# Performance work log

Hardware: AMD Instinct MI355X
Metric: run time of the kernel (lower is better)

The kernel has to match this reference:

```python
import jax, jax.numpy as jnp
import numpy as np

B, N, DIN, DOUT, EIN, EOUT = 8, 256, 64, 64, 64, 64


def setup_inputs() -> dict:
    key = jax.random.key(0)
    ks = jax.random.split(key, 9)
    A = jax.random.randint(ks[0], (B, N, N), 0, 2).astype(jnp.float32)  # {0,1} connectivity
    emb_node = jax.random.normal(ks[1], (B, N, DIN), dtype=jnp.float32)
    emb_edge = jax.random.normal(ks[2], (B, N, N, EIN), dtype=jnp.float32)
    s_n = 1.0 / np.sqrt(DIN)
    s_e = 1.0 / np.sqrt(EIN)
    Wn = jax.random.uniform(ks[3], (DIN, DOUT), minval=-s_n, maxval=s_n)
    bn = jax.random.uniform(ks[4], (DOUT,), minval=-s_n, maxval=s_n)
    Wsn = jax.random.uniform(ks[5], (DIN, DOUT), minval=-s_n, maxval=s_n)
    bsn = jax.random.uniform(ks[6], (DOUT,), minval=-s_n, maxval=s_n)
    We = jax.random.uniform(ks[7], (EIN, EOUT), minval=-s_e, maxval=s_e)
    be = jax.random.uniform(ks[8], (EOUT,), minval=-s_e, maxval=s_e)
    return {"A": A, "emb_node": emb_node, "emb_edge": emb_edge,
            "Wn": Wn, "bn": bn, "Wsn": Wsn, "bsn": bsn, "We": We, "be": be}


def reference(A, emb_node, emb_edge, Wn, bn, Wsn, bsn, We, be):
    # mode=1 (default) of ChannelIndependentConv
    node_x = emb_node @ Wn + bn          # [B,N,DOUT]
    node_sx = emb_node @ Wsn + bsn       # [B,N,DOUT]
    edge_x = emb_edge @ We + be          # [B,N,N,EOUT]
    # mask edges by connectivity, then channel-independent aggregation:
    # out[b,i,c] = sum_j A[b,i,j] * edge_x[b,i,j,c] * node_x[b,j,c]
    Ae = A[..., None] * edge_x           # [B,N,N,EOUT]
    agg = jnp.einsum('bijc,bjc->bic', Ae, node_x)  # [B,N,DOUT]
    node_out = jax.nn.relu(agg) + jax.nn.relu(node_sx)
    edge_out = jax.nn.relu(edge_x)
    return node_out, edge_out
```

## Files before the change

kernel.cpp:

```cpp
#include <hip/hip_runtime.h>
#include <hip/hip_bf16.h>

#define BN   2048
#define NN   256
#define CH   64

typedef __attribute__((ext_vector_type(8))) short short8;
typedef __attribute__((ext_vector_type(4))) float fv4;

static __device__ inline short f2bf(float f) {
  unsigned u = __float_as_uint(f);
  u += 0x7FFF + ((u >> 16) & 1);
  return (short)(u >> 16);
}
static __device__ inline short8 cvt8(fv4 a, fv4 b) {
  short8 f;
  f[0] = f2bf(a[0]); f[1] = f2bf(a[1]); f[2] = f2bf(a[2]); f[3] = f2bf(a[3]);
  f[4] = f2bf(b[0]); f[5] = f2bf(b[1]); f[6] = f2bf(b[2]); f[7] = f2bf(b[3]);
  return f;
}

__global__ __launch_bounds__(256) void node_kernel(
    const float* __restrict__ emb_node, const float* __restrict__ Wn,
    const float* __restrict__ bn, const float* __restrict__ Wsn,
    const float* __restrict__ bsn, float* __restrict__ node_x,
    float* __restrict__ rsx) {
  __shared__ float s_emb[4][CH];
  __shared__ float s_Wn[CH * CH];
  __shared__ float s_Ws[CH * CH];
  const int tid = threadIdx.x;
  const int r = tid >> 6;
  const int c = tid & 63;
  const int row = blockIdx.x * 4 + r;
#pragma unroll
  for (int i = 0; i < 4; ++i) {
    *(fv4*)&s_Wn[(i * 256 + tid) * 4] = *(const fv4*)&Wn[(i * 256 + tid) * 4];
    *(fv4*)&s_Ws[(i * 256 + tid) * 4] = *(const fv4*)&Wsn[(i * 256 + tid) * 4];
  }
  s_emb[r][c] = emb_node[row * CH + c];
  __syncthreads();
  float a1 = bn[c], a2 = bsn[c];
#pragma unroll
  for (int k = 0; k < CH; ++k) {
    const float e = s_emb[r][k];
    a1 = fmaf(e, s_Wn[k * CH + c], a1);
    a2 = fmaf(e, s_Ws[k * CH + c], a2);
  }
  node_x[row * CH + c] = a1;
  rsx[row * CH + c] = fmaxf(a2, 0.0f);
}

__global__ __launch_bounds__(256) void edge_mfma_kernel(
    const float* __restrict__ A, const float* __restrict__ emb_edge,
    const float* __restrict__ We, const float* __restrict__ be,
    const float* __restrict__ node_x, const float* __restrict__ rsx,
    float* __restrict__ node_out, float* __restrict__ edge_out) {
  const int bi   = blockIdx.x;
  const int b    = bi >> 8;
  const int tid  = threadIdx.x;
  const int lane = tid & 63;
  const int wave = tid >> 6;
  const int l15  = lane & 15;
  const int quad = lane >> 4;

  __shared__ float s_A[NN];
  __shared__ float s_agg[CH];

  s_A[tid] = A[(size_t)bi * NN + tid];
  if (tid < CH) s_agg[tid] = 0.0f;

  short8 bfrag[4][2];
  float bias[4];
#pragma unroll
  for (int ct = 0; ct < 4; ++ct) {
    const int c = 16 * ct + l15;
#pragma unroll
    for (int h = 0; h < 2; ++h)
#pragma unroll
      for (int j = 0; j < 8; ++j)
        bfrag[ct][h][j] = f2bf(We[(h * 32 + quad * 8 + j) * CH + c]);
    bias[ct] = be[c];
  }

  const float* __restrict__ ee = emb_edge + (size_t)bi * NN * CH;
  float*       __restrict__ eo = edge_out + (size_t)bi * NN * CH;
  const float* __restrict__ nx = node_x + (size_t)b * NN * CH;

  const int jbase = wave * 64;
  __syncthreads();

  fv4 ld[2][4];
#pragma unroll
  for (int q = 0; q < 4; ++q) {
    const float* p = ee + (size_t)(jbase + l15) * CH + quad * 8 + (q & 1) * 4 + (q >> 1) * 32;
    ld[0][q] = __builtin_nontemporal_load((const fv4*)p);
  }

  float agg[4] = {0.0f, 0.0f, 0.0f, 0.0f};

#pragma unroll
  for (int t = 0; t < 4; ++t) {
    const int pb = t & 1;
    if (t < 3) {
#pragma unroll
      for (int q = 0; q < 4; ++q) {
        const float* p = ee + (size_t)(jbase + (t + 1) * 16 + l15) * CH +
                         quad * 8 + (q & 1) * 4 + (q >> 1) * 32;
        ld[pb ^ 1][q] = __builtin_nontemporal_load((const fv4*)p);
      }
    }
    const int rbase = jbase + t * 16 + quad * 4;
    float nxv[4][4];
#pragma unroll
    for (int ct = 0; ct < 4; ++ct)
#pragma unroll
      for (int r = 0; r < 4; ++r)
        nxv[ct][r] = nx[(rbase + r) * CH + 16 * ct + l15];

    const short8 af0 = cvt8(ld[pb][0], ld[pb][1]);
    const short8 af1 = cvt8(ld[pb][2], ld[pb][3]);
    fv4 acc[4];
#pragma unroll
    for (int ct = 0; ct < 4; ++ct) {
      acc[ct] = fv4{0.0f, 0.0f, 0.0f, 0.0f};
      acc[ct] = __builtin_amdgcn_mfma_f32_16x16x32_bf16(af0, bfrag[ct][0], acc[ct], 0, 0, 0);
      acc[ct] = __builtin_amdgcn_mfma_f32_16x16x32_bf16(af1, bfrag[ct][1], acc[ct], 0, 0, 0);
    }

    const fv4 av = *(const fv4*)&s_A[rbase];
#pragma unroll
    for (int ct = 0; ct < 4; ++ct) {
      const int c = 16 * ct + l15;
#pragma unroll
      for (int r = 0; r < 4; ++r) {
        const float ex = acc[ct][r] + bias[ct];
        __builtin_nontemporal_store(fmaxf(ex, 0.0f), eo + (rbase + r) * CH + c);
        agg[ct] = fmaf(av[r] * ex, nxv[ct][r], agg[ct]);
      }
    }
  }

#pragma unroll
  for (int ct = 0; ct < 4; ++ct) {
    agg[ct] += __shfl_xor(agg[ct], 16, 64);
    agg[ct] += __shfl_xor(agg[ct], 32, 64);
  }
  if (quad == 0) {
#pragma unroll
    for (int ct = 0; ct < 4; ++ct)
      atomicAdd(&s_agg[16 * ct + l15], agg[ct]);
  }
  __syncthreads();
  if (tid < CH) {
    node_out[(size_t)bi * CH + tid] =
        fmaxf(s_agg[tid], 0.0f) + rsx[(size_t)bi * CH + tid];
  }
}

extern "C" void kernel_launch(void* const* d_in, const int* in_sizes, int n_in,
                              void* d_out, int out_size, void* d_ws, size_t ws_size,
                              hipStream_t stream) {
  const float* A        = (const float*)d_in[0];
  const float* emb_node = (const float*)d_in[1];
  const float* emb_edge = (const float*)d_in[2];
  const float* Wn       = (const float*)d_in[3];
  const float* bn       = (const float*)d_in[4];
  const float* Wsn      = (const float*)d_in[5];
  const float* bsn      = (const float*)d_in[6];
  const float* We       = (const float*)d_in[7];
  const float* be       = (const float*)d_in[8];

  float* node_out = (float*)d_out;
  float* edge_out = (float*)d_out + (size_t)BN * CH;

  float* node_x = (float*)d_ws;
  float* rsx    = (float*)d_ws + (size_t)BN * CH;

  hipLaunchKernelGGL(node_kernel, dim3(BN / 4), dim3(256), 0, stream,
                     emb_node, Wn, bn, Wsn, bsn, node_x, rsx);
  hipLaunchKernelGGL(edge_mfma_kernel, dim3(BN), dim3(256), 0, stream,
                     A, emb_edge, We, be, node_x, rsx, node_out, edge_out);
}
```

Before: 269.0 us.

## Deepen edge load prefetch, hoist loads before weight setup, and truncate bf16 via perm

Issues the first two 16-row tiles of edge embeddings and the first node_x tile before the We/bias fragment setup and the barrier, so more memory traffic is in flight early. The edge prefetch distance grows from one tile to two, and node_x rows are double-buffered one tile ahead. The float-to-bf16 conversion switches from round-to-nearest-even to byte-permute truncation, which uses fewer ALU ops but loses the rounding step and slightly lowers accuracy. Register use goes up with the extra buffers.

```diff
diff --git a/kernel.cpp b/kernel.cpp
--- a/kernel.cpp
+++ b/kernel.cpp
@@ -13,11 +13,14 @@
   u += 0x7FFF + ((u >> 16) & 1);
   return (short)(u >> 16);
 }
-static __device__ inline short8 cvt8(fv4 a, fv4 b) {
-  short8 f;
-  f[0] = f2bf(a[0]); f[1] = f2bf(a[1]); f[2] = f2bf(a[2]); f[3] = f2bf(a[3]);
-  f[4] = f2bf(b[0]); f[5] = f2bf(b[1]); f[6] = f2bf(b[2]); f[7] = f2bf(b[3]);
-  return f;
+
+static __device__ inline short8 pk8(fv4 a, fv4 b) {
+  union { short8 s; unsigned u[4]; } r;
+  r.u[0] = __builtin_amdgcn_perm(__float_as_uint(a[1]), __float_as_uint(a[0]), 0x07060302u);
+  r.u[1] = __builtin_amdgcn_perm(__float_as_uint(a[3]), __float_as_uint(a[2]), 0x07060302u);
+  r.u[2] = __builtin_amdgcn_perm(__float_as_uint(b[1]), __float_as_uint(b[0]), 0x07060302u);
+  r.u[3] = __builtin_amdgcn_perm(__float_as_uint(b[3]), __float_as_uint(b[2]), 0x07060302u);
+  return r.s;
 }
 
 __global__ __launch_bounds__(256) void node_kernel(
@@ -69,6 +72,28 @@
   s_A[tid] = A[(size_t)bi * NN + tid];
   if (tid < CH) s_agg[tid] = 0.0f;
 
+  const float* __restrict__ ee = emb_edge + (size_t)bi * NN * CH;
+  float*       __restrict__ eo = edge_out + (size_t)bi * NN * CH;
+  const float* __restrict__ nx = node_x + (size_t)b * NN * CH;
+  const int jbase = wave * 64;
+
+  fv4 ld[4][4];
+#pragma unroll
+  for (int t = 0; t < 2; ++t)
+#pragma unroll
+    for (int q = 0; q < 4; ++q) {
+      const float* p = ee + (size_t)(jbase + t * 16 + l15) * CH +
+                       quad * 8 + (q & 1) * 4 + (q >> 1) * 32;
+      ld[t][q] = __builtin_nontemporal_load((const fv4*)p);
+    }
+
+  float nxv[2][4][4];
+#pragma unroll
+  for (int ct = 0; ct < 4; ++ct)
+#pragma unroll
+    for (int r = 0; r < 4; ++r)
+      nxv[0][ct][r] = nx[(jbase + quad * 4 + r) * CH + 16 * ct + l15];
+
   short8 bfrag[4][2];
   float bias[4];
 #pragma unroll
@@ -82,43 +107,30 @@
     bias[ct] = be[c];
   }
 
-  const float* __restrict__ ee = emb_edge + (size_t)bi * NN * CH;
-  float*       __restrict__ eo = edge_out + (size_t)bi * NN * CH;
-  const float* __restrict__ nx = node_x + (size_t)b * NN * CH;
-
-  const int jbase = wave * 64;
+  float agg[4] = {0.0f, 0.0f, 0.0f, 0.0f};
   __syncthreads();
-
-  fv4 ld[2][4];
-#pragma unroll
-  for (int q = 0; q < 4; ++q) {
-    const float* p = ee + (size_t)(jbase + l15) * CH + quad * 8 + (q & 1) * 4 + (q >> 1) * 32;
-    ld[0][q] = __builtin_nontemporal_load((const fv4*)p);
-  }
-
-  float agg[4] = {0.0f, 0.0f, 0.0f, 0.0f};
 
 #pragma unroll
   for (int t = 0; t < 4; ++t) {
-    const int pb = t & 1;
-    if (t < 3) {
+    if (t < 2) {
 #pragma unroll
       for (int q = 0; q < 4; ++q) {
-        const float* p = ee + (size_t)(jbase + (t + 1) * 16 + l15) * CH +
+        const float* p = ee + (size_t)(jbase + (t + 2) * 16 + l15) * CH +
                          quad * 8 + (q & 1) * 4 + (q >> 1) * 32;
-        ld[pb ^ 1][q] = __builtin_nontemporal_load((const fv4*)p);
+        ld[t + 2][q] = __builtin_nontemporal_load((const fv4*)p);
       }
     }
-    const int rbase = jbase + t * 16 + quad * 4;
-    float nxv[4][4];
+    if (t < 3) {
+      const int rb1 = jbase + (t + 1) * 16 + quad * 4;
 #pragma unroll
-    for (int ct = 0; ct < 4; ++ct)
+      for (int ct = 0; ct < 4; ++ct)
 #pragma unroll
-      for (int r = 0; r < 4; ++r)
-        nxv[ct][r] = nx[(rbase + r) * CH + 16 * ct + l15];
+        for (int r = 0; r < 4; ++r)
+          nxv[(t + 1) & 1][ct][r] = nx[(rb1 + r) * CH + 16 * ct + l15];
+    }
 
-    const short8 af0 = cvt8(ld[pb][0], ld[pb][1]);
-    const short8 af1 = cvt8(ld[pb][2], ld[pb][3]);
+    const short8 af0 = pk8(ld[t][0], ld[t][1]);
+    const short8 af1 = pk8(ld[t][2], ld[t][3]);
     fv4 acc[4];
 #pragma unroll
     for (int ct = 0; ct < 4; ++ct) {
@@ -127,6 +139,7 @@
       acc[ct] = __builtin_amdgcn_mfma_f32_16x16x32_bf16(af1, bfrag[ct][1], acc[ct], 0, 0, 0);
     }
 
+    const int rbase = jbase + t * 16 + quad * 4;
     const fv4 av = *(const fv4*)&s_A[rbase];
 #pragma unroll
     for (int ct = 0; ct < 4; ++ct) {
@@ -135,7 +148,7 @@
       for (int r = 0; r < 4; ++r) {
         const float ex = acc[ct][r] + bias[ct];
         __builtin_nontemporal_store(fmaxf(ex, 0.0f), eo + (rbase + r) * CH + c);
-        agg[ct] = fmaf(av[r] * ex, nxv[ct][r], agg[ct]);
+        agg[ct] = fmaf(av[r] * ex, nxv[t & 1][ct][r], agg[ct]);
       }
     }
   }
```

Measured after the change: 268.3 us. No clear change (-0.3%).
